# Kernel optimization log

Measured on AMD Instinct MI355X. Metric: run time of the kernel, lower is better.

## Reference

```python
import jax, jax.numpy as jnp
import numpy as np

MARGIN = 0.3
N = 8192
D = 128
NUM_CLASSES = 256

def setup_inputs() -> dict:
    key = jax.random.key(0)
    k1, k2 = jax.random.split(key)
    inputs = jax.random.normal(k1, (N, D), dtype=jnp.float32)
    targets = jax.random.randint(k2, (N,), 0, NUM_CLASSES, dtype=jnp.int64)
    return {"inputs": inputs, "targets": targets}

def reference(inputs, targets):
    n = inputs.shape[0]
    dt = inputs.dtype
    # pairwise euclidean distances: ||xi||^2 + ||xj||^2 - 2 xi.xj, clamped and sqrt'ed
    sq = jnp.sum(inputs * inputs, axis=1)                     # [n]
    d2 = sq[:, None] + sq[None, :] - 2.0 * (inputs @ inputs.T)
    dist = jnp.sqrt(jnp.clip(d2, 1e-12, None))                # [n, n]
    dsq = dist * dist                                         # squared dists used by the loss

    mask = targets[:, None] == targets[None, :]               # same-identity mask [n, n]

    # positives: torch code sorts and drops the smallest (the self-distance ~1e-6)
    pos_d = jnp.where(mask, dist, jnp.inf)
    min_idx = jnp.argmin(pos_d, axis=1)                       # index of dropped element per row
    excl = jnp.arange(n)[None, :] == min_idx[:, None]
    pos_valid = mask & ~excl                                  # remaining positives
    cnt_p = jnp.sum(pos_valid, axis=1).astype(dt)
    sigma_p = jnp.sum(jnp.where(pos_valid, dsq, 0.0), axis=1) / cnt_p
    max_p = jnp.max(jnp.where(pos_valid, dsq, -jnp.inf), axis=1)
    dist_ap = max_p / sigma_p + 0.5 * jnp.log(sigma_p)        # [n]

    # negatives: all different-identity entries
    neg = ~mask
    cnt_n = jnp.sum(neg, axis=1).astype(dt)
    sigma_n = jnp.sum(jnp.where(neg, dsq, 0.0), axis=1) / cnt_n
    min_n = jnp.min(jnp.where(neg, dsq, jnp.inf), axis=1)
    dist_an = min_n / sigma_n + 0.5 * jnp.log(sigma_n)        # [n]

    # MarginRankingLoss with y=1: mean(max(0, -(an - ap) + margin))
    loss = jnp.mean(jnp.maximum(dist_ap - dist_an + MARGIN, 0.0))
    return loss
```

## Files before the change

### kernel.cpp

```cpp
#include <hip/hip_runtime.h>
#include <math.h>


#define NROWS 8192
#define MARGIN_F 0.3f

typedef short bf16x8 __attribute__((ext_vector_type(8)));
typedef float f32x16 __attribute__((ext_vector_type(16)));
union U4B { uint4 u; bf16x8 h; };

__device__ __forceinline__ unsigned short f2bf(float x) {
    unsigned u = __float_as_uint(x);
    return (unsigned short)((u + 0x7fffu + ((u >> 16) & 1u)) >> 16);
}

__global__ __launch_bounds__(256) void prep_kernel(const float* __restrict__ X,
                                                   const int* __restrict__ tgt,
                                                   float* __restrict__ sq,
                                                   int* __restrict__ bh) {
    __shared__ int lh[256];
    int tid = threadIdx.x;
    lh[tid] = 0;
    __syncthreads();
    if (blockIdx.x < 64 && tid < 128)
        atomicAdd(&lh[tgt[blockIdx.x * 128 + tid]], 1);
    int w = tid >> 6, l = tid & 63;
    int row0 = blockIdx.x * 32;
    #pragma unroll
    for (int i = 0; i < 8; ++i) {
        int r = row0 + w * 8 + i;
        float2 v = ((const float2*)X)[(size_t)r * 64 + l];
        float s = v.x * v.x + v.y * v.y;
        for (int d = 32; d > 0; d >>= 1) s += __shfl_down(s, d, 64);
        if (l == 0) sq[r] = s;
    }
    __syncthreads();
    if (blockIdx.x < 64) bh[blockIdx.x * 256 + tid] = lh[tid];
}

__global__ __launch_bounds__(256) void offsets_kernel(const int* __restrict__ bh,
                                                      const int* __restrict__ tgt,
                                                      const float* __restrict__ sq,
                                                      int* __restrict__ hist,
                                                      int* __restrict__ offg,
                                                      int* __restrict__ boff,
                                                      float* __restrict__ S_class,
                                                      float* __restrict__ S_all) {
    __shared__ int sh[256];
    __shared__ float scl[256];
    __shared__ float red[4];
    int c = threadIdx.x;
    int h = 0;
    for (int b = 0; b < 64; ++b) h += bh[b * 256 + c];
    hist[c] = h;
    sh[c] = h;
    scl[c] = 0.0f;
    __syncthreads();
    for (int d = 1; d < 256; d <<= 1) {
        int t = (c >= d) ? sh[c - d] : 0;
        __syncthreads();
        sh[c] += t;
        __syncthreads();
    }
    int off = sh[c] - h;
    offg[c] = off;
    for (int i = 0; i < 32; ++i) {
        int r = i * 256 + c;
        atomicAdd(&scl[tgt[r]], sq[r]);
    }
    __syncthreads();
    float sc = scl[c];
    S_class[c] = sc;
    float t2 = sc;
    for (int d = 32; d > 0; d >>= 1) t2 += __shfl_down(t2, d, 64);
    if ((c & 63) == 0) red[c >> 6] = t2;
    __syncthreads();
    if (c == 0) S_all[0] = red[0] + red[1] + red[2] + red[3];
    int run = off;
    for (int b = 0; b < 64; ++b) {
        boff[b * 256 + c] = run;
        run += bh[b * 256 + c];
    }
}

__global__ __launch_bounds__(256) void scatter_kernel(
        const float* __restrict__ X, const int* __restrict__ tgt,
        const float* __restrict__ sq, const int* __restrict__ hist,
        const int* __restrict__ offg, const int* __restrict__ boff,
        unsigned short* __restrict__ Xs, float* __restrict__ u_s,
        int* __restrict__ cls_s, int* __restrict__ csA, int* __restrict__ wdA) {
    __shared__ int cur[256];
    __shared__ int pos_sh[128];
    int tid = threadIdx.x;
    cur[tid] = boff[blockIdx.x * 256 + tid];
    __syncthreads();
    int row0 = blockIdx.x * 128;
    if (tid < 128) {
        int c = tgt[row0 + tid];
        int p = atomicAdd(&cur[c], 1);
        pos_sh[tid] = p;
        u_s[p] = 0.5f * sq[row0 + tid];
        cls_s[p] = c;
        csA[p] = offg[c];
        wdA[p] = hist[c];
    }
    __syncthreads();
    int w = tid >> 6, l = tid & 63;
    #pragma unroll 4
    for (int i = 0; i < 32; ++i) {
        int rl = w * 32 + i;
        int p = pos_sh[rl];
        float2 v = ((const float2*)X)[(size_t)(row0 + rl) * 64 + l];
        ushort2 h2;
        h2.x = f2bf(v.x);
        h2.y = f2bf(v.y);
        ((ushort2*)Xs)[(size_t)p * 64 + l] = h2;
    }
}

__global__ __launch_bounds__(256, 2) void dist_kernel(
        const unsigned short* __restrict__ Xs, const float* __restrict__ u_s,
        const int* __restrict__ csA, const int* __restrict__ wdA,
        float4* __restrict__ partial, int ns_mask, int jb_shift, int tiles) {
    __shared__ uint4 As[128 * 16];
    __shared__ float ush[128];
    const int tid = threadIdx.x;
    const int w = tid >> 6, l = tid & 63, hl = l >> 5, l31 = l & 31;
    const int bx = blockIdx.x;
    const int slice = bx & ns_mask;
    const int jb = bx >> jb_shift;

    {
        const uint4* src = (const uint4*)Xs + (size_t)jb * 128 * 16;
        #pragma unroll
        for (int s = 0; s < 8; ++s) {
            int g = s * 256 + tid, row = g >> 4, c = g & 15;
            As[row * 16 + (c ^ (row & 15))] = src[g];
        }
    }
    __syncthreads();
    bf16x8 Bf[4][8];
    int cs[4], wd[4];
    #pragma unroll
    for (int ct = 0; ct < 4; ++ct) {
        int colb = ct * 32 + l31;
        cs[ct] = csA[jb * 128 + colb];
        wd[ct] = wdA[jb * 128 + colb];
        #pragma unroll
        for (int kk = 0; kk < 8; ++kk) {
            U4B t; t.u = As[colb * 16 + ((kk * 2 + hl) ^ (colb & 15))];
            Bf[ct][kk] = t.h;
        }
    }

    float Sa[4] = {0.f, 0.f, 0.f, 0.f};
    float Ss[4] = {0.f, 0.f, 0.f, 0.f};
    float Mp[4] = {-INFINITY, -INFINITY, -INFINITY, -INFINITY};
    float Mn[4] = { INFINITY,  INFINITY,  INFINITY,  INFINITY};

    for (int t = 0; t < tiles; ++t) {
        const int i0 = (slice * tiles + t) * 128;
        __syncthreads();
        {
            const uint4* src = (const uint4*)Xs + (size_t)i0 * 16;
            #pragma unroll
            for (int s = 0; s < 8; ++s) {
                int g = s * 256 + tid, row = g >> 4, c = g & 15;
                As[row * 16 + (c ^ (row & 15))] = src[g];
            }
            if (tid < 128) ush[tid] = u_s[i0 + tid];
        }
        __syncthreads();

        float ur[16];
        #pragma unroll
        for (int r = 0; r < 16; ++r)
            ur[r] = ush[w * 32 + (r & 3) + 8 * (r >> 2) + 4 * hl];

        f32x16 acc[4];
        #pragma unroll
        for (int ct = 0; ct < 4; ++ct) acc[ct] = (f32x16)0.0f;
        const int arow = w * 32 + l31;
        #pragma unroll
        for (int kk = 0; kk < 8; ++kk) {
            U4B a; a.u = As[arow * 16 + ((kk * 2 + hl) ^ (arow & 15))];
            #pragma unroll
            for (int ct = 0; ct < 4; ++ct)
                acc[ct] = __builtin_amdgcn_mfma_f32_32x32x16_bf16(a.h, Bf[ct][kk], acc[ct], 0, 0, 0);
        }

        const int rowb = i0 + w * 32 + 4 * hl;
        #pragma unroll
        for (int ct = 0; ct < 4; ++ct) {
            bool bl = (cs[ct] < i0 + 128) && (cs[ct] + wd[ct] > i0);
            if (__any(bl)) {
                int tb = rowb - cs[ct];
                unsigned wdu = (unsigned)wd[ct];
                #pragma unroll
                for (int r = 0; r < 16; ++r) {
                    float a = acc[ct][r];
                    float v = ur[r] - a;
                    bool in = (unsigned)(tb + (r & 3) + 8 * (r >> 2)) < wdu;
                    Sa[ct] += a;
                    Ss[ct] += in ? a : 0.0f;
                    Mp[ct] = fmaxf(Mp[ct], in ? v : -INFINITY);
                    Mn[ct] = in ? Mn[ct] : fminf(Mn[ct], v);
                }
            } else {
                #pragma unroll
                for (int r = 0; r < 16; r += 2) {
                    float a1 = acc[ct][r], a2 = acc[ct][r + 1];
                    float v1 = ur[r] - a1, v2 = ur[r + 1] - a2;
                    Mn[ct] = fminf(Mn[ct], fminf(v1, v2));
                    Sa[ct] += (a1 + a2);
                }
            }
        }
    }

    #pragma unroll
    for (int ct = 0; ct < 4; ++ct) {
        Sa[ct] += __shfl_xor(Sa[ct], 32, 64);
        Ss[ct] += __shfl_xor(Ss[ct], 32, 64);
        Mp[ct] = fmaxf(Mp[ct], __shfl_xor(Mp[ct], 32, 64));
        Mn[ct] = fminf(Mn[ct], __shfl_xor(Mn[ct], 32, 64));
    }
    __syncthreads();
    float4* sm = (float4*)As;
    if (l < 32) {
        #pragma unroll
        for (int ct = 0; ct < 4; ++ct)
            sm[(ct * 32 + l31) * 4 + w] = make_float4(Sa[ct], Ss[ct], Mp[ct], Mn[ct]);
    }
    __syncthreads();
    if (tid < 128) {
        float4 a = sm[tid * 4 + 0], b = sm[tid * 4 + 1];
        float4 c2 = sm[tid * 4 + 2], d = sm[tid * 4 + 3];
        float4 o;
        o.x = a.x + b.x + c2.x + d.x;
        o.y = a.y + b.y + c2.y + d.y;
        o.z = fmaxf(fmaxf(a.z, b.z), fmaxf(c2.z, d.z));
        o.w = fminf(fminf(a.w, b.w), fminf(c2.w, d.w));
        partial[(size_t)slice * NROWS + jb * 128 + tid] = o;
    }
}

__global__ __launch_bounds__(256) void combine_kernel(
        const float* __restrict__ u_s, const int* __restrict__ cls_s,
        const int* __restrict__ wdA, const float* __restrict__ S_class,
        const float* __restrict__ S_all, const float4* __restrict__ partial,
        float* __restrict__ blocksum, int ns) {
    int tid = threadIdx.x;
    int j = blockIdx.x * 256 + tid;
    float Sa = 0.f, Ss = 0.f, Mp = -INFINITY, Mn = INFINITY;
    for (int s = 0; s < ns; ++s) {
        float4 p = partial[(size_t)s * NROWS + j];
        Sa += p.x; Ss += p.y;
        Mp = fmaxf(Mp, p.z); Mn = fminf(Mn, p.w);
    }
    float sqj = 2.0f * u_s[j];
    int c = cls_s[j];
    float cnt = (float)wdA[j];
    float sumall = (float)NROWS * sqj + S_all[0] - 2.0f * Sa;
    float sump = cnt * sqj + S_class[c] - 2.0f * Ss;
    float sumn = sumall - sump;
    float sigp = sump / (cnt - 1.0f);
    float sign_ = sumn / ((float)NROWS - cnt);
    float ap = (sqj + 2.0f * Mp) / sigp + 0.5f * __logf(sigp);
    float an = (sqj + 2.0f * Mn) / sign_ + 0.5f * __logf(sign_);
    float h = fmaxf(ap - an + MARGIN_F, 0.0f);
    for (int d = 32; d > 0; d >>= 1) h += __shfl_down(h, d, 64);
    __shared__ float hs[4];
    int l = tid & 63, w = tid >> 6;
    if (l == 0) hs[w] = h;
    __syncthreads();
    if (tid == 0) blocksum[blockIdx.x] = hs[0] + hs[1] + hs[2] + hs[3];
}

__global__ __launch_bounds__(64) void final_kernel(const float* __restrict__ blocksum,
                                                   float* __restrict__ out) {
    int tid = threadIdx.x;
    float s = (tid < 32) ? blocksum[tid] : 0.0f;
    for (int d = 32; d > 0; d >>= 1) s += __shfl_down(s, d, 64);
    if (tid == 0) out[0] = s * (1.0f / NROWS);
}

extern "C" void kernel_launch(void* const* d_in, const int* in_sizes, int n_in,
                              void* d_out, int out_size, void* d_ws, size_t ws_size,
                              hipStream_t stream) {
    const float* X = (const float*)d_in[0];
    const int* tgt = (const int*)d_in[1];
    float* out = (float*)d_out;

    float* f = (float*)d_ws;
    int*   hist    = (int*)f;
    int*   offg    = (int*)(f + 256);
    float* S_class = f + 512;
    float* S_all   = f + 768;
    int*   bh      = (int*)(f + 1024);
    int*   boff    = (int*)(f + 17408);
    float* sq      = f + 33792;
    float* u_s     = f + 41984;
    int*   cls_s   = (int*)(f + 50176);
    int*   csA     = (int*)(f + 58368);
    int*   wdA     = (int*)(f + 66560);
    float* blocksum = f + 74752;
    unsigned short* Xs = (unsigned short*)(f + 74784);
    float4* partial = (float4*)(f + 599072);

    int ns = 16;
    while (ns > 2 && ws_size < ((size_t)599072 + (size_t)ns * NROWS * 4) * sizeof(float))
        ns >>= 1;
    int shift = (ns == 16) ? 4 : (ns == 8) ? 3 : 2;
    int tiles = 64 / ns;

    prep_kernel<<<256, 256, 0, stream>>>(X, tgt, sq, bh);
    offsets_kernel<<<1, 256, 0, stream>>>(bh, tgt, sq, hist, offg, boff, S_class, S_all);
    scatter_kernel<<<64, 256, 0, stream>>>(X, tgt, sq, hist, offg, boff, Xs, u_s,
                                           cls_s, csA, wdA);
    dist_kernel<<<64 * ns, 256, 0, stream>>>(Xs, u_s, csA, wdA, partial,
                                             ns - 1, shift, tiles);
    combine_kernel<<<32, 256, 0, stream>>>(u_s, cls_s, wdA, S_class, S_all,
                                           partial, blocksum, ns);
    final_kernel<<<1, 64, 0, stream>>>(blocksum, out);
}
```

Measured before the change: 130.8 us.

## Drop class sorting; pack class id into norm bits for same-class masking

Removes the histogram/offset/scatter pipeline that sorted rows by class. Instead, the class id is packed into the low 8 mantissa bits of the half-norm, and every tile entry is masked by comparing those bits against the column's class. This cuts two kernel launches and the scatter pass. In exchange, the fast path that skipped masking for tiles with no same-class rows is gone, so every element does the full masked update. The column block is halved to 64 with triple occupancy and double the grid, and per-class counts and sums now use global atomics after a memset; the packed low bits slightly perturb the norm.

Measured after the change: 119.9 us. 8.3% less time.

```diff
diff --git a/kernel.cpp b/kernel.cpp
--- a/kernel.cpp
+++ b/kernel.cpp
@@ -17,111 +17,43 @@
 __global__ __launch_bounds__(256) void prep_kernel(const float* __restrict__ X,
                                                    const int* __restrict__ tgt,
                                                    float* __restrict__ sq,
-                                                   int* __restrict__ bh) {
-    __shared__ int lh[256];
-    int tid = threadIdx.x;
-    lh[tid] = 0;
-    __syncthreads();
-    if (blockIdx.x < 64 && tid < 128)
-        atomicAdd(&lh[tgt[blockIdx.x * 128 + tid]], 1);
-    int w = tid >> 6, l = tid & 63;
-    int row0 = blockIdx.x * 32;
+                                                   float* __restrict__ upk,
+                                                   unsigned short* __restrict__ Xbf,
+                                                   int* __restrict__ hist,
+                                                   float* __restrict__ S_class,
+                                                   float* __restrict__ bsum) {
+    int tid = threadIdx.x, w = tid >> 6, l = tid & 63;
+    int row0 = blockIdx.x * 32 + w * 8;
+    float rs = 0.0f;
     #pragma unroll
     for (int i = 0; i < 8; ++i) {
-        int r = row0 + w * 8 + i;
+        int r = row0 + i;
         float2 v = ((const float2*)X)[(size_t)r * 64 + l];
-        float s = v.x * v.x + v.y * v.y;
-        for (int d = 32; d > 0; d >>= 1) s += __shfl_down(s, d, 64);
-        if (l == 0) sq[r] = s;
-    }
-    __syncthreads();
-    if (blockIdx.x < 64) bh[blockIdx.x * 256 + tid] = lh[tid];
-}
-
-__global__ __launch_bounds__(256) void offsets_kernel(const int* __restrict__ bh,
-                                                      const int* __restrict__ tgt,
-                                                      const float* __restrict__ sq,
-                                                      int* __restrict__ hist,
-                                                      int* __restrict__ offg,
-                                                      int* __restrict__ boff,
-                                                      float* __restrict__ S_class,
-                                                      float* __restrict__ S_all) {
-    __shared__ int sh[256];
-    __shared__ float scl[256];
-    __shared__ float red[4];
-    int c = threadIdx.x;
-    int h = 0;
-    for (int b = 0; b < 64; ++b) h += bh[b * 256 + c];
-    hist[c] = h;
-    sh[c] = h;
-    scl[c] = 0.0f;
-    __syncthreads();
-    for (int d = 1; d < 256; d <<= 1) {
-        int t = (c >= d) ? sh[c - d] : 0;
-        __syncthreads();
-        sh[c] += t;
-        __syncthreads();
-    }
-    int off = sh[c] - h;
-    offg[c] = off;
-    for (int i = 0; i < 32; ++i) {
-        int r = i * 256 + c;
-        atomicAdd(&scl[tgt[r]], sq[r]);
-    }
-    __syncthreads();
-    float sc = scl[c];
-    S_class[c] = sc;
-    float t2 = sc;
-    for (int d = 32; d > 0; d >>= 1) t2 += __shfl_down(t2, d, 64);
-    if ((c & 63) == 0) red[c >> 6] = t2;
-    __syncthreads();
-    if (c == 0) S_all[0] = red[0] + red[1] + red[2] + red[3];
-    int run = off;
-    for (int b = 0; b < 64; ++b) {
-        boff[b * 256 + c] = run;
-        run += bh[b * 256 + c];
-    }
-}
-
-__global__ __launch_bounds__(256) void scatter_kernel(
-        const float* __restrict__ X, const int* __restrict__ tgt,
-        const float* __restrict__ sq, const int* __restrict__ hist,
-        const int* __restrict__ offg, const int* __restrict__ boff,
-        unsigned short* __restrict__ Xs, float* __restrict__ u_s,
-        int* __restrict__ cls_s, int* __restrict__ csA, int* __restrict__ wdA) {
-    __shared__ int cur[256];
-    __shared__ int pos_sh[128];
-    int tid = threadIdx.x;
-    cur[tid] = boff[blockIdx.x * 256 + tid];
-    __syncthreads();
-    int row0 = blockIdx.x * 128;
-    if (tid < 128) {
-        int c = tgt[row0 + tid];
-        int p = atomicAdd(&cur[c], 1);
-        pos_sh[tid] = p;
-        u_s[p] = 0.5f * sq[row0 + tid];
-        cls_s[p] = c;
-        csA[p] = offg[c];
-        wdA[p] = hist[c];
-    }
-    __syncthreads();
-    int w = tid >> 6, l = tid & 63;
-    #pragma unroll 4
-    for (int i = 0; i < 32; ++i) {
-        int rl = w * 32 + i;
-        int p = pos_sh[rl];
-        float2 v = ((const float2*)X)[(size_t)(row0 + rl) * 64 + l];
         ushort2 h2;
         h2.x = f2bf(v.x);
         h2.y = f2bf(v.y);
-        ((ushort2*)Xs)[(size_t)p * 64 + l] = h2;
-    }
-}
-
-__global__ __launch_bounds__(256, 2) void dist_kernel(
-        const unsigned short* __restrict__ Xs, const float* __restrict__ u_s,
-        const int* __restrict__ csA, const int* __restrict__ wdA,
-        float4* __restrict__ partial, int ns_mask, int jb_shift, int tiles) {
+        ((ushort2*)Xbf)[(size_t)r * 64 + l] = h2;
+        float s = v.x * v.x + v.y * v.y;
+        for (int d = 32; d > 0; d >>= 1) s += __shfl_down(s, d, 64);
+        if (l == 0) {
+            sq[r] = s;
+            rs += s;
+            int c = tgt[r];
+            upk[r] = __uint_as_float((__float_as_uint(0.5f * s) & 0xffffff00u) | (unsigned)c);
+            atomicAdd(&hist[c], 1);
+            atomicAdd(&S_class[c], s);
+        }
+    }
+    __shared__ float bs[4];
+    if (l == 0) bs[w] = rs;
+    __syncthreads();
+    if (tid == 0) bsum[blockIdx.x] = bs[0] + bs[1] + bs[2] + bs[3];
+}
+
+__global__ __launch_bounds__(256, 3) void dist_kernel(
+        const unsigned short* __restrict__ Xbf, const int* __restrict__ tgt,
+        const float* __restrict__ upk, float4* __restrict__ partial,
+        int ns_mask, int jb_shift, int tiles) {
     __shared__ uint4 As[128 * 16];
     __shared__ float ush[128];
     const int tid = threadIdx.x;
@@ -131,21 +63,20 @@
     const int jb = bx >> jb_shift;
 
     {
-        const uint4* src = (const uint4*)Xs + (size_t)jb * 128 * 16;
-        #pragma unroll
-        for (int s = 0; s < 8; ++s) {
+        const uint4* src = (const uint4*)Xbf + (size_t)jb * 64 * 16;
+        #pragma unroll
+        for (int s = 0; s < 4; ++s) {
             int g = s * 256 + tid, row = g >> 4, c = g & 15;
             As[row * 16 + (c ^ (row & 15))] = src[g];
         }
     }
     __syncthreads();
-    bf16x8 Bf[4][8];
-    int cs[4], wd[4];
+    bf16x8 Bf[2][8];
+    int tjt[2];
     #pragma unroll
-    for (int ct = 0; ct < 4; ++ct) {
+    for (int ct = 0; ct < 2; ++ct) {
         int colb = ct * 32 + l31;
-        cs[ct] = csA[jb * 128 + colb];
-        wd[ct] = wdA[jb * 128 + colb];
+        tjt[ct] = tgt[jb * 64 + colb];
         #pragma unroll
         for (int kk = 0; kk < 8; ++kk) {
             U4B t; t.u = As[colb * 16 + ((kk * 2 + hl) ^ (colb & 15))];
@@ -153,22 +84,22 @@
         }
     }
 
-    float Sa[4] = {0.f, 0.f, 0.f, 0.f};
-    float Ss[4] = {0.f, 0.f, 0.f, 0.f};
-    float Mp[4] = {-INFINITY, -INFINITY, -INFINITY, -INFINITY};
-    float Mn[4] = { INFINITY,  INFINITY,  INFINITY,  INFINITY};
+    float Sa[2] = {0.f, 0.f};
+    float Ss[2] = {0.f, 0.f};
+    float Mp[2] = {-INFINITY, -INFINITY};
+    float Mn[2] = { INFINITY,  INFINITY};
 
     for (int t = 0; t < tiles; ++t) {
         const int i0 = (slice * tiles + t) * 128;
         __syncthreads();
         {
-            const uint4* src = (const uint4*)Xs + (size_t)i0 * 16;
+            const uint4* src = (const uint4*)Xbf + (size_t)i0 * 16;
             #pragma unroll
             for (int s = 0; s < 8; ++s) {
                 int g = s * 256 + tid, row = g >> 4, c = g & 15;
                 As[row * 16 + (c ^ (row & 15))] = src[g];
             }
-            if (tid < 128) ush[tid] = u_s[i0 + tid];
+            if (tid < 128) ush[tid] = upk[i0 + tid];
         }
         __syncthreads();
 
@@ -177,49 +108,35 @@
         for (int r = 0; r < 16; ++r)
             ur[r] = ush[w * 32 + (r & 3) + 8 * (r >> 2) + 4 * hl];
 
-        f32x16 acc[4];
-        #pragma unroll
-        for (int ct = 0; ct < 4; ++ct) acc[ct] = (f32x16)0.0f;
+        f32x16 acc[2];
+        acc[0] = (f32x16)0.0f;
+        acc[1] = (f32x16)0.0f;
         const int arow = w * 32 + l31;
         #pragma unroll
         for (int kk = 0; kk < 8; ++kk) {
             U4B a; a.u = As[arow * 16 + ((kk * 2 + hl) ^ (arow & 15))];
+            acc[0] = __builtin_amdgcn_mfma_f32_32x32x16_bf16(a.h, Bf[0][kk], acc[0], 0, 0, 0);
+            acc[1] = __builtin_amdgcn_mfma_f32_32x32x16_bf16(a.h, Bf[1][kk], acc[1], 0, 0, 0);
+        }
+
+        #pragma unroll
+        for (int ct = 0; ct < 2; ++ct) {
+            const int tt = tjt[ct];
             #pragma unroll
-            for (int ct = 0; ct < 4; ++ct)
-                acc[ct] = __builtin_amdgcn_mfma_f32_32x32x16_bf16(a.h, Bf[ct][kk], acc[ct], 0, 0, 0);
-        }
-
-        const int rowb = i0 + w * 32 + 4 * hl;
-        #pragma unroll
-        for (int ct = 0; ct < 4; ++ct) {
-            bool bl = (cs[ct] < i0 + 128) && (cs[ct] + wd[ct] > i0);
-            if (__any(bl)) {
-                int tb = rowb - cs[ct];
-                unsigned wdu = (unsigned)wd[ct];
-                #pragma unroll
-                for (int r = 0; r < 16; ++r) {
-                    float a = acc[ct][r];
-                    float v = ur[r] - a;
-                    bool in = (unsigned)(tb + (r & 3) + 8 * (r >> 2)) < wdu;
-                    Sa[ct] += a;
-                    Ss[ct] += in ? a : 0.0f;
-                    Mp[ct] = fmaxf(Mp[ct], in ? v : -INFINITY);
-                    Mn[ct] = in ? Mn[ct] : fminf(Mn[ct], v);
-                }
-            } else {
-                #pragma unroll
-                for (int r = 0; r < 16; r += 2) {
-                    float a1 = acc[ct][r], a2 = acc[ct][r + 1];
-                    float v1 = ur[r] - a1, v2 = ur[r + 1] - a2;
-                    Mn[ct] = fminf(Mn[ct], fminf(v1, v2));
-                    Sa[ct] += (a1 + a2);
-                }
+            for (int r = 0; r < 16; ++r) {
+                float a = acc[ct][r];
+                float v = ur[r] - a;
+                bool same = ((__float_as_int(ur[r]) & 0xff) == tt);
+                Sa[ct] += a;
+                Ss[ct] += same ? a : 0.0f;
+                Mp[ct] = fmaxf(Mp[ct], same ? v : -INFINITY);
+                Mn[ct] = same ? Mn[ct] : fminf(Mn[ct], v);
             }
         }
     }
 
     #pragma unroll
-    for (int ct = 0; ct < 4; ++ct) {
+    for (int ct = 0; ct < 2; ++ct) {
         Sa[ct] += __shfl_xor(Sa[ct], 32, 64);
         Ss[ct] += __shfl_xor(Ss[ct], 32, 64);
         Mp[ct] = fmaxf(Mp[ct], __shfl_xor(Mp[ct], 32, 64));
@@ -229,11 +146,11 @@
     float4* sm = (float4*)As;
     if (l < 32) {
         #pragma unroll
-        for (int ct = 0; ct < 4; ++ct)
+        for (int ct = 0; ct < 2; ++ct)
             sm[(ct * 32 + l31) * 4 + w] = make_float4(Sa[ct], Ss[ct], Mp[ct], Mn[ct]);
     }
     __syncthreads();
-    if (tid < 128) {
+    if (tid < 64) {
         float4 a = sm[tid * 4 + 0], b = sm[tid * 4 + 1];
         float4 c2 = sm[tid * 4 + 2], d = sm[tid * 4 + 3];
         float4 o;
@@ -241,16 +158,25 @@
         o.y = a.y + b.y + c2.y + d.y;
         o.z = fmaxf(fmaxf(a.z, b.z), fmaxf(c2.z, d.z));
         o.w = fminf(fminf(a.w, b.w), fminf(c2.w, d.w));
-        partial[(size_t)slice * NROWS + jb * 128 + tid] = o;
+        partial[(size_t)slice * NROWS + jb * 64 + tid] = o;
     }
 }
 
 __global__ __launch_bounds__(256) void combine_kernel(
-        const float* __restrict__ u_s, const int* __restrict__ cls_s,
-        const int* __restrict__ wdA, const float* __restrict__ S_class,
-        const float* __restrict__ S_all, const float4* __restrict__ partial,
+        const float* __restrict__ sq, const int* __restrict__ tgt,
+        const int* __restrict__ hist, const float* __restrict__ S_class,
+        const float* __restrict__ bsum, const float4* __restrict__ partial,
         float* __restrict__ blocksum, int ns) {
-    int tid = threadIdx.x;
+    __shared__ float red[4];
+    __shared__ float hs[4];
+    int tid = threadIdx.x, l = tid & 63, w = tid >> 6;
+
+    float b = bsum[tid];
+    for (int d = 32; d > 0; d >>= 1) b += __shfl_down(b, d, 64);
+    if (l == 0) red[w] = b;
+    __syncthreads();
+    float S_all = red[0] + red[1] + red[2] + red[3];
+
     int j = blockIdx.x * 256 + tid;
     float Sa = 0.f, Ss = 0.f, Mp = -INFINITY, Mn = INFINITY;
     for (int s = 0; s < ns; ++s) {
@@ -258,10 +184,10 @@
         Sa += p.x; Ss += p.y;
         Mp = fmaxf(Mp, p.z); Mn = fminf(Mn, p.w);
     }
-    float sqj = 2.0f * u_s[j];
-    int c = cls_s[j];
-    float cnt = (float)wdA[j];
-    float sumall = (float)NROWS * sqj + S_all[0] - 2.0f * Sa;
+    float sqj = sq[j];
+    int c = tgt[j];
+    float cnt = (float)hist[c];
+    float sumall = (float)NROWS * sqj + S_all - 2.0f * Sa;
     float sump = cnt * sqj + S_class[c] - 2.0f * Ss;
     float sumn = sumall - sump;
     float sigp = sump / (cnt - 1.0f);
@@ -270,8 +196,6 @@
     float an = (sqj + 2.0f * Mn) / sign_ + 0.5f * __logf(sign_);
     float h = fmaxf(ap - an + MARGIN_F, 0.0f);
     for (int d = 32; d > 0; d >>= 1) h += __shfl_down(h, d, 64);
-    __shared__ float hs[4];
-    int l = tid & 63, w = tid >> 6;
     if (l == 0) hs[w] = h;
     __syncthreads();
     if (tid == 0) blocksum[blockIdx.x] = hs[0] + hs[1] + hs[2] + hs[3];
@@ -293,34 +217,26 @@
     float* out = (float*)d_out;
 
     float* f = (float*)d_ws;
-    int*   hist    = (int*)f;
-    int*   offg    = (int*)(f + 256);
-    float* S_class = f + 512;
-    float* S_all   = f + 768;
-    int*   bh      = (int*)(f + 1024);
-    int*   boff    = (int*)(f + 17408);
-    float* sq      = f + 33792;
-    float* u_s     = f + 41984;
-    int*   cls_s   = (int*)(f + 50176);
-    int*   csA     = (int*)(f + 58368);
-    int*   wdA     = (int*)(f + 66560);
-    float* blocksum = f + 74752;
-    unsigned short* Xs = (unsigned short*)(f + 74784);
-    float4* partial = (float4*)(f + 599072);
+    int*   hist     = (int*)f;
+    float* S_class  = f + 256;
+    float* bsum     = f + 512;
+    float* blocksum = f + 768;
+    float* sq       = f + 1024;
+    float* upk      = f + 9216;
+    unsigned short* Xbf = (unsigned short*)(f + 17408);
+    float4* partial = (float4*)(f + 541696);
 
     int ns = 16;
-    while (ns > 2 && ws_size < ((size_t)599072 + (size_t)ns * NROWS * 4) * sizeof(float))
+    while (ns > 2 && ws_size < ((size_t)541696 + (size_t)ns * NROWS * 4) * sizeof(float))
         ns >>= 1;
     int shift = (ns == 16) ? 4 : (ns == 8) ? 3 : 2;
     int tiles = 64 / ns;
 
-    prep_kernel<<<256, 256, 0, stream>>>(X, tgt, sq, bh);
-    offsets_kernel<<<1, 256, 0, stream>>>(bh, tgt, sq, hist, offg, boff, S_class, S_all);
-    scatter_kernel<<<64, 256, 0, stream>>>(X, tgt, sq, hist, offg, boff, Xs, u_s,
-                                           cls_s, csA, wdA);
-    dist_kernel<<<64 * ns, 256, 0, stream>>>(Xs, u_s, csA, wdA, partial,
-                                             ns - 1, shift, tiles);
-    combine_kernel<<<32, 256, 0, stream>>>(u_s, cls_s, wdA, S_class, S_all,
+    hipMemsetAsync(d_ws, 0, 2048, stream);
+    prep_kernel<<<256, 256, 0, stream>>>(X, tgt, sq, upk, Xbf, hist, S_class, bsum);
+    dist_kernel<<<128 * ns, 256, 0, stream>>>(Xbf, tgt, upk, partial,
+                                              ns - 1, shift, tiles);
+    combine_kernel<<<32, 256, 0, stream>>>(sq, tgt, hist, S_class, bsum,
                                            partial, blocksum, ns);
     final_kernel<<<1, 64, 0, stream>>>(blocksum, out);
 }
```
